# Performance work log

Measured on AMD Instinct MI355X. Metric: run time of the kernel, lower is better.

## Reference

```python
import jax, jax.numpy as jnp
import numpy as np

N = 100000      # nodes
E = 1600000     # edges (avg degree 16)
F_IN = 64       # num_features
HID = 16        # hidden channels (fixed in module)
OUT = 32        # num_classes
K = 2           # kernel_size (dim=1, degree=1 open B-spline -> 2 basis fns)


def setup_inputs() -> dict:
    key = jax.random.key(0)
    ks = jax.random.split(key, 8)
    return {
        "x": jax.random.normal(ks[0], (N, F_IN), jnp.float32),
        "edge_index": jax.random.randint(ks[1], (2, E), 0, N, dtype=jnp.int64),
        "dropout": 0,  # unused in eval mode (F.dropout training=False)
        "edge_attr": jnp.full((E, 1), 0.1, jnp.float32),  # nt([0.1]) broadcast per edge
        "W1": jax.random.normal(ks[2], (K, F_IN, HID), jnp.float32) / np.sqrt(K * F_IN).astype(np.float32),
        "root1": jax.random.normal(ks[3], (F_IN, HID), jnp.float32) / np.sqrt(F_IN).astype(np.float32),
        "bias1": jnp.zeros((HID,), jnp.float32),
        "W2": jax.random.normal(ks[4], (K, HID, OUT), jnp.float32) / np.sqrt(K * HID).astype(np.float32),
        "root2": jax.random.normal(ks[5], (HID, OUT), jnp.float32) / np.sqrt(HID).astype(np.float32),
        "bias2": jnp.zeros((OUT,), jnp.float32),
    }


def spline_conv(x, edge_index, edge_attr, W, root, bias):
    """SplineConv, dim=1, kernel_size=2, degree=1 open B-spline, aggr='mean'."""
    src, dst = edge_index[0], edge_index[1]
    n = x.shape[0]
    u = edge_attr[:, 0]                                  # [E] pseudo-coords in [0,1]
    # degree-1 open spline, kernel_size=2: frac = u*(ks-1) = u; kernels {0,1}
    basis = jnp.stack([1.0 - u, u], axis=1)              # [E, K]
    # transform at node level (cheaper than gathering raw features per edge)
    h = jnp.einsum('nf,kfo->nko', x, W)                  # [N, K, out]
    msg = jnp.einsum('ek,eko->eo', basis, h[src])        # [E, out]
    summed = jax.ops.segment_sum(msg, dst, num_segments=n)
    deg = jax.ops.segment_sum(jnp.ones_like(u), dst, num_segments=n)
    out = summed / jnp.maximum(deg, 1.0)[:, None]        # mean aggregation
    return out + x @ root + bias                          # root weight + bias


def reference(x, edge_index, dropout, edge_attr, W1, root1, bias1, W2, root2, bias2):
    # dropout is a no-op in eval mode
    h = jax.nn.elu(spline_conv(x, edge_index, edge_attr, W1, root1, bias1))
    h = spline_conv(h, edge_index, edge_attr, W2, root2, bias2)
    return jax.nn.log_softmax(h, axis=1)
```

## Files before the change

### kernel.cpp

```cpp
#include <hip/hip_runtime.h>
#include <math.h>

#define NN 100000
#define NE 1600000
#define F_IN 64
#define HID 16
#define OUTF 32
#define BKT_SHIFT 6
#define BKT_NODES 64
#define NBKT 1563
#define SRCM 0x1FFFF
#define CAP_REG 2048
#define CAP_LDS 1536
#define PBLK2 512
#define EPB2 (NE / PBLK2)
#define OVF_MAX 4096

__device__ __forceinline__ unsigned bf16r(float f) {
    unsigned u = __float_as_uint(f);
    return (u + 0x7FFFu + ((u >> 16) & 1u)) >> 16;
}
__device__ __forceinline__ float bfa(unsigned p) { return __uint_as_float(p << 16); }
__device__ __forceinline__ float bfd(unsigned p) { return __uint_as_float(p & 0xFFFF0000u); }
__device__ __forceinline__ float bfh(unsigned short v) { return __uint_as_float(((unsigned)v) << 16); }

__global__ __launch_bounds__(256) void zeroG_kernel(int* __restrict__ gcur,
                                                    int* __restrict__ novf) {
    int t = blockIdx.x * 256 + threadIdx.x;
    if (t < NBKT) gcur[t] = 0;
    if (t == NBKT) novf[0] = 0;
}

__global__ __launch_bounds__(1024) void partF_kernel(const int* __restrict__ ei,
                                                     const float* __restrict__ ea,
                                                     int* __restrict__ gcur,
                                                     int* __restrict__ novf,
                                                     int4* __restrict__ ovf,
                                                     int2* __restrict__ bkt) {
    __shared__ int hcnt[NBKT];
    __shared__ int hbase[NBKT];
    __shared__ int lbase[NBKT];
    __shared__ int s[1024];
    __shared__ int2 sbuf[EPB2];
    __shared__ unsigned short bid[EPB2];
    int t = threadIdx.x, blk = blockIdx.x;
    for (int i = t; i < NBKT; i += 1024) hcnt[i] = 0;
    __syncthreads();
    int beg = blk * EPB2, end = beg + EPB2;
    for (int e = beg + t; e < end; e += 1024)
        atomicAdd(&hcnt[ei[NE + e] >> BKT_SHIFT], 1);
    __syncthreads();
    int i0 = 2 * t, i1 = 2 * t + 1;
    int v0 = (i0 < NBKT) ? hcnt[i0] : 0;
    int v1 = (i1 < NBKT) ? hcnt[i1] : 0;
    s[t] = v0 + v1;
    __syncthreads();
    for (int off = 1; off < 1024; off <<= 1) {
        int xv = (t >= off) ? s[t - off] : 0;
        __syncthreads();
        s[t] += xv;
        __syncthreads();
    }
    int run = (t == 0) ? 0 : s[t - 1];
    if (i0 < NBKT) lbase[i0] = run;
    if (i1 < NBKT) lbase[i1] = run + v0;
    __syncthreads();
    for (int i = t; i < NBKT; i += 1024) {
        int c = hcnt[i];
        hbase[i] = c ? atomicAdd(&gcur[i], c) : 0;
        hcnt[i] = 0;
    }
    __syncthreads();
    for (int e = beg + t; e < end; e += 1024) {
        int src = ei[e];
        int dst = ei[NE + e];
        float u = ea[e];
        int b = dst >> BKT_SHIFT;
        int r = atomicAdd(&hcnt[b], 1);
        int lp = lbase[b] + r;
        sbuf[lp] = make_int2(src | ((dst & (BKT_NODES - 1)) << 17), __float_as_int(u));
        bid[lp] = (unsigned short)b;
    }
    __syncthreads();
    for (int i = t; i < EPB2; i += 1024) {
        int2 pk = sbuf[i];
        int b = bid[i];
        int p = hbase[b] + (i - lbase[b]);
        if (p < CAP_REG) {
            bkt[(size_t)b * CAP_REG + p] = pk;
        } else {
            int o = atomicAdd(novf, 1);
            if (o < OVF_MAX)
                ovf[o] = make_int4(b * BKT_NODES + (pk.x >> 17), pk.x & SRCM, pk.y, 0);
        }
    }
}

__global__ __launch_bounds__(256) void proj1_kernel(const float* __restrict__ x,
                                                    const float* __restrict__ W1,
                                                    const float* __restrict__ root1,
                                                    const float* __restrict__ bias1,
                                                    unsigned* __restrict__ ab1p,
                                                    float* __restrict__ r1) {
    __shared__ float w[2 * F_IN * HID];
    __shared__ float wr[F_IN * HID];
    __shared__ float bb[HID];
    for (int i = threadIdx.x; i < 2 * F_IN * HID; i += 256) w[i] = W1[i];
    for (int i = threadIdx.x; i < F_IN * HID; i += 256) wr[i] = root1[i];
    if (threadIdx.x < HID) bb[threadIdx.x] = bias1[threadIdx.x];
    __syncthreads();
    int n = blockIdx.x * 256 + threadIdx.x;
    if (n >= NN) return;
    float accA[HID], accB[HID], accR[HID];
#pragma unroll
    for (int o = 0; o < HID; ++o) { accA[o] = 0.f; accB[o] = 0.f; accR[o] = bb[o]; }
    const float* xr = x + (size_t)n * F_IN;
    for (int f = 0; f < F_IN; ++f) {
        float xv = xr[f];
        const float* w0 = &w[f * HID];
        const float* w1 = &w[F_IN * HID + f * HID];
        const float* w2 = &wr[f * HID];
#pragma unroll
        for (int o = 0; o < HID; ++o) {
            accA[o] = fmaf(xv, w0[o], accA[o]);
            accB[o] = fmaf(xv, w1[o], accB[o]);
            accR[o] = fmaf(xv, w2[o], accR[o]);
        }
    }
    unsigned* ar = ab1p + (size_t)n * HID;
    float* rr = r1 + (size_t)n * HID;
#pragma unroll
    for (int o = 0; o < HID; ++o) {
        ar[o] = bf16r(accA[o]) | (bf16r(accB[o] - accA[o]) << 16);
        rr[o] = accR[o];
    }
}

__global__ __launch_bounds__(512) void gather1_kernel(const int* __restrict__ gcur,
                                                      const int* __restrict__ novf,
                                                      const int4* __restrict__ ovf,
                                                      int2* __restrict__ bkt,
                                                      const unsigned* __restrict__ ab1p,
                                                      const float* __restrict__ r1,
                                                      unsigned short* __restrict__ h16,
                                                      float* __restrict__ dinv,
                                                      int* __restrict__ segg) {
    __shared__ int2 raw[CAP_LDS];
    __shared__ int2 sorted[CAP_LDS];
    __shared__ int cnt[BKT_NODES], cur[BKT_NODES], segb[BKT_NODES + 1];
    __shared__ float degsL[BKT_NODES];
    int t = threadIdx.x;
    int b = blockIdx.x;
    int tot = gcur[b];
    int beg = b * CAP_REG;
    if (t < BKT_NODES) { cnt[t] = 0; cur[t] = 0; degsL[t] = 0.f; }
    __syncthreads();
    int nodeBase = b * BKT_NODES;

    if (tot <= CAP_LDS) {
        for (int e = t; e < tot; e += 512) raw[e] = bkt[beg + e];
        __syncthreads();
        for (int e = t; e < tot; e += 512)
            atomicAdd(&cnt[((unsigned)raw[e].x) >> 17], 1);
        __syncthreads();
        if (t < BKT_NODES) {
            int v = cnt[t];
            int sc = v;
#pragma unroll
            for (int off = 1; off < 64; off <<= 1) {
                int o = __shfl_up(sc, off, 64);
                if (t >= off) sc += o;
            }
            segb[t] = sc - v;
            if (t == 63) segb[64] = sc;
        }
        __syncthreads();
        for (int e = t; e < tot; e += 512) {
            int2 pk = raw[e];
            int loc = ((unsigned)pk.x) >> 17;
            int pos = segb[loc] + atomicAdd(&cur[loc], 1);
            sorted[pos] = pk;
        }
        __syncthreads();
        for (int e = t; e < tot; e += 512) bkt[beg + e] = sorted[e];
        if (t <= BKT_NODES) segg[b * (BKT_NODES + 1) + t] = segb[t];
        int j = t & (HID - 1);
        int g = t >> 4;
        int s = segb[2 * g], mid = segb[2 * g + 1], e2 = segb[2 * g + 2];
        float a0 = 0.f, a1 = 0.f;
        int e = s;
        for (; e + 8 <= mid; e += 8) {
            float val[8];
#pragma unroll
            for (int k = 0; k < 8; ++k) {
                int2 pk = sorted[e + k];
                unsigned p = ab1p[(size_t)(pk.x & SRCM) * HID + j];
                val[k] = fmaf(__int_as_float(pk.y), bfd(p), bfa(p));
            }
#pragma unroll
            for (int k = 0; k < 8; ++k) a0 += val[k];
        }
        for (; e < mid; ++e) {
            int2 pk = sorted[e];
            unsigned p = ab1p[(size_t)(pk.x & SRCM) * HID + j];
            a0 += fmaf(__int_as_float(pk.y), bfd(p), bfa(p));
        }
        for (; e + 8 <= e2; e += 8) {
            float val[8];
#pragma unroll
            for (int k = 0; k < 8; ++k) {
                int2 pk = sorted[e + k];
                unsigned p = ab1p[(size_t)(pk.x & SRCM) * HID + j];
                val[k] = fmaf(__int_as_float(pk.y), bfd(p), bfa(p));
            }
#pragma unroll
            for (int k = 0; k < 8; ++k) a1 += val[k];
        }
        for (; e < e2; ++e) {
            int2 pk = sorted[e];
            unsigned p = ab1p[(size_t)(pk.x & SRCM) * HID + j];
            a1 += fmaf(__int_as_float(pk.y), bfd(p), bfa(p));
        }
        float d0 = 1.f / (float)max(mid - s, 1);
        float d1 = 1.f / (float)max(e2 - mid, 1);
        int n0 = nodeBase + 2 * g, n1 = n0 + 1;
        if (n0 < NN) {
            float v = a0 * d0 + r1[(size_t)n0 * HID + j];
            h16[(size_t)n0 * HID + j] = (unsigned short)bf16r(v > 0.f ? v : expm1f(v));
            if (j == 0) dinv[n0] = d0;
        }
        if (n1 < NN) {
            float v = a1 * d1 + r1[(size_t)n1 * HID + j];
            h16[(size_t)n1 * HID + j] = (unsigned short)bf16r(v > 0.f ? v : expm1f(v));
            if (j == 0) dinv[n1] = d1;
        }
    } else {
        float* accL = (float*)raw;
        int inreg = min(tot, CAP_REG);
        int end = beg + inreg;
        for (int i = t; i < BKT_NODES * HID; i += 512) accL[i] = 0.f;
        __syncthreads();
        int j = t & (HID - 1);
        int g = t >> 4;
        for (int e = beg + g; e < end; e += 32) {
            int2 pk = bkt[e];
            unsigned p = ab1p[(size_t)(pk.x & SRCM) * HID + j];
            atomicAdd(&accL[(((unsigned)pk.x) >> 17) * HID + j],
                      fmaf(__int_as_float(pk.y), bfd(p), bfa(p)));
            if (j == 0) atomicAdd(&degsL[((unsigned)pk.x) >> 17], 1.f);
        }
        int ovn = min(novf[0], OVF_MAX);
        for (int o = 0; o < ovn; ++o) {
            int4 ent = ovf[o];
            int loc = ent.x - nodeBase;
            if (loc >= 0 && loc < BKT_NODES && g == 0) {
                unsigned p = ab1p[(size_t)ent.y * HID + j];
                atomicAdd(&accL[loc * HID + j], fmaf(__int_as_float(ent.z), bfd(p), bfa(p)));
                if (j == 0) atomicAdd(&degsL[loc], 1.f);
            }
        }
        __syncthreads();
        if (t < BKT_NODES) degsL[t] = 1.f / fmaxf(degsL[t], 1.f);
        if (t == 0) segg[b * (BKT_NODES + 1)] = -1;
        __syncthreads();
#pragma unroll
        for (int it = 0; it < BKT_NODES * HID / 512; ++it) {
            int idx = it * 512 + t;
            int nl = idx >> 4, jj = idx & (HID - 1);
            int n = nodeBase + nl;
            if (n < NN) {
                float v = accL[idx] * degsL[nl] + r1[(size_t)n * HID + jj];
                h16[(size_t)n * HID + jj] = (unsigned short)bf16r(v > 0.f ? v : expm1f(v));
            }
        }
        if (t < BKT_NODES && nodeBase + t < NN) dinv[nodeBase + t] = degsL[t];
    }
}

__global__ __launch_bounds__(512) void gather2_kernel(const int* __restrict__ gcur,
                                                      const int* __restrict__ novf,
                                                      const int4* __restrict__ ovf,
                                                      const int2* __restrict__ bkt,
                                                      const unsigned short* __restrict__ h16,
                                                      const float* __restrict__ W2,
                                                      const float* __restrict__ root2,
                                                      const float* __restrict__ bias2,
                                                      const float* __restrict__ dinv,
                                                      const int* __restrict__ segg,
                                                      float* __restrict__ out) {
    __shared__ int2 sbufL[CAP_LDS];
    __shared__ int segb[BKT_NODES + 1];
    __shared__ float s0L[BKT_NODES * HID];
    __shared__ float s1L[BKT_NODES * HID];
    __shared__ float w20[HID * OUTF], w2d[HID * OUTF], wr[HID * OUTF];
    __shared__ float bb[OUTF];
    int t = threadIdx.x;
    for (int i = t; i < HID * OUTF; i += 512) {
        float a = W2[i];
        w20[i] = a;
        w2d[i] = W2[HID * OUTF + i] - a;
        wr[i] = root2[i];
    }
    if (t < OUTF) bb[t] = bias2[t];
    int b = blockIdx.x;
    int tot = gcur[b];
    int beg = b * CAP_REG;
    int nodeBase = b * BKT_NODES;
    if (t <= BKT_NODES) segb[t] = segg[b * (BKT_NODES + 1) + t];
    __syncthreads();

    if (tot <= CAP_LDS && segb[0] != -1) {
        for (int e = t; e < tot; e += 512) sbufL[e] = bkt[beg + e];
        __syncthreads();
        int j = t & (HID - 1);
        int g = t >> 4;
        int s = segb[2 * g], mid = segb[2 * g + 1], e2 = segb[2 * g + 2];
        float s00 = 0.f, s10 = 0.f, s01 = 0.f, s11 = 0.f;
        int e = s;
        for (; e + 8 <= mid; e += 8) {
            float hv[8], uv[8];
#pragma unroll
            for (int k = 0; k < 8; ++k) {
                int2 pk = sbufL[e + k];
                hv[k] = bfh(h16[(size_t)(pk.x & SRCM) * HID + j]);
                uv[k] = __int_as_float(pk.y);
            }
#pragma unroll
            for (int k = 0; k < 8; ++k) {
                s00 += hv[k];
                s10 = fmaf(uv[k], hv[k], s10);
            }
        }
        for (; e < mid; ++e) {
            int2 pk = sbufL[e];
            float hvv = bfh(h16[(size_t)(pk.x & SRCM) * HID + j]);
            s00 += hvv;
            s10 = fmaf(__int_as_float(pk.y), hvv, s10);
        }
        for (; e + 8 <= e2; e += 8) {
            float hv[8], uv[8];
#pragma unroll
            for (int k = 0; k < 8; ++k) {
                int2 pk = sbufL[e + k];
                hv[k] = bfh(h16[(size_t)(pk.x & SRCM) * HID + j]);
                uv[k] = __int_as_float(pk.y);
            }
#pragma unroll
            for (int k = 0; k < 8; ++k) {
                s01 += hv[k];
                s11 = fmaf(uv[k], hv[k], s11);
            }
        }
        for (; e < e2; ++e) {
            int2 pk = sbufL[e];
            float hvv = bfh(h16[(size_t)(pk.x & SRCM) * HID + j]);
            s01 += hvv;
            s11 = fmaf(__int_as_float(pk.y), hvv, s11);
        }
        s0L[(2 * g) * HID + j] = s00;
        s1L[(2 * g) * HID + j] = s10;
        s0L[(2 * g + 1) * HID + j] = s01;
        s1L[(2 * g + 1) * HID + j] = s11;
        __syncthreads();
    } else {
        int inreg = min(tot, CAP_REG);
        int end = beg + inreg;
        for (int i = t; i < BKT_NODES * HID; i += 512) { s0L[i] = 0.f; s1L[i] = 0.f; }
        __syncthreads();
        int j = t & (HID - 1);
        int g = t >> 4;
        for (int e = beg + g; e < end; e += 32) {
            int2 pk = bkt[e];
            float hvv = bfh(h16[(size_t)(pk.x & SRCM) * HID + j]);
            int l = ((unsigned)pk.x) >> 17;
            atomicAdd(&s0L[l * HID + j], hvv);
            atomicAdd(&s1L[l * HID + j], __int_as_float(pk.y) * hvv);
        }
        int ovn = min(novf[0], OVF_MAX);
        for (int o = 0; o < ovn; ++o) {
            int4 ent = ovf[o];
            int loc = ent.x - nodeBase;
            if (loc >= 0 && loc < BKT_NODES && g == 0) {
                float hvv = bfh(h16[(size_t)ent.y * HID + j]);
                atomicAdd(&s0L[loc * HID + j], hvv);
                atomicAdd(&s1L[loc * HID + j], __int_as_float(ent.z) * hvv);
            }
        }
        __syncthreads();
    }

#pragma unroll
    for (int it = 0; it < BKT_NODES * OUTF / 512; ++it) {
        int idx = it * 512 + t;
        int nl = idx >> 5, jj = idx & (OUTF - 1);
        int n = nodeBase + nl;
        float v = 0.f;
        if (n < NN) {
            float msum = 0.f;
            const float* S0 = &s0L[nl * HID];
            const float* S1 = &s1L[nl * HID];
#pragma unroll
            for (int f = 0; f < HID; ++f)
                msum += S0[f] * w20[f * OUTF + jj] + S1[f] * w2d[f * OUTF + jj];
            v = msum * dinv[n] + bb[jj];
            const unsigned short* hr = h16 + (size_t)n * HID;
#pragma unroll
            for (int f = 0; f < HID; ++f)
                v = fmaf(bfh(hr[f]), wr[f * OUTF + jj], v);
        }
        float m = v;
#pragma unroll
        for (int mask = 16; mask >= 1; mask >>= 1) m = fmaxf(m, __shfl_xor(m, mask));
        float ex = expf(v - m);
        float sm = ex;
#pragma unroll
        for (int mask = 16; mask >= 1; mask >>= 1) sm += __shfl_xor(sm, mask);
        if (n < NN) out[(size_t)n * OUTF + jj] = v - m - logf(sm);
    }
}

extern "C" void kernel_launch(void* const* d_in, const int* in_sizes, int n_in,
                              void* d_out, int out_size, void* d_ws, size_t ws_size,
                              hipStream_t stream) {
    const float* x     = (const float*)d_in[0];
    const int*   ei    = (const int*)d_in[1];
    const float* ea    = (const float*)d_in[3];
    const float* W1    = (const float*)d_in[4];
    const float* root1 = (const float*)d_in[5];
    const float* bias1 = (const float*)d_in[6];
    const float* W2    = (const float*)d_in[7];
    const float* root2 = (const float*)d_in[8];
    const float* bias2 = (const float*)d_in[9];
    float* out = (float*)d_out;
    float* ws  = (float*)d_ws;

    const size_t N = NN;
    int*            gcur = (int*)(ws);
    int*            novf = (int*)(ws + 2000);
    int4*           ovf  = (int4*)(ws + 2048);
    float*          dinv = ws + 20000;
    int*            segg = (int*)(ws + 120000);
    float*          r1   = ws + 222000;
    unsigned*       ab1p = (unsigned*)(ws + 222000 + 16 * N);
    unsigned short* h16  = (unsigned short*)(ws + 222000 + 32 * N);
    int2*           bkt  = (int2*)(ws + 222000 + 40 * N);

    int nbN = (NN + 255) / 256;
    zeroG_kernel<<<(NBKT + 256) / 256, 256, 0, stream>>>(gcur, novf);
    partF_kernel<<<PBLK2, 1024, 0, stream>>>(ei, ea, gcur, novf, ovf, bkt);
    proj1_kernel<<<nbN, 256, 0, stream>>>(x, W1, root1, bias1, ab1p, r1);
    gather1_kernel<<<NBKT, 512, 0, stream>>>(gcur, novf, ovf, bkt, ab1p, r1, h16, dinv, segg);
    gather2_kernel<<<NBKT, 512, 0, stream>>>(gcur, novf, ovf, bkt, h16, W2, root2, bias2, dinv, segg, out);
}
```

Before: 127.3 us.

## Vectorize edge loads and gathers, remap threads to per-node lanes

Partition blocks now use 500 blocks of 3200 edges so each thread loads four edges with int4/float4 vector reads. The projection kernel reads x rows as float4. Both gather kernels are remapped so that groups of 8 threads cover one node and each thread loads 4 or 8 packed bf16 features per edge as uint4, then combines partial sums with shuffles. Layer-2 self features are staged in LDS once per bucket. The aim is fewer, wider memory transactions on the irregular gathers, at the cost of shuffle reductions and possible lane imbalance on nodes with few edges.

```diff
diff --git a/kernel.cpp b/kernel.cpp
--- a/kernel.cpp
+++ b/kernel.cpp
@@ -12,8 +12,8 @@
 #define SRCM 0x1FFFF
 #define CAP_REG 2048
 #define CAP_LDS 1536
-#define PBLK2 512
-#define EPB2 (NE / PBLK2)
+#define PBLK2 500
+#define EPB2 3200
 #define OVF_MAX 4096
 
 __device__ __forceinline__ unsigned bf16r(float f) {
@@ -23,6 +23,23 @@
 __device__ __forceinline__ float bfa(unsigned p) { return __uint_as_float(p << 16); }
 __device__ __forceinline__ float bfd(unsigned p) { return __uint_as_float(p & 0xFFFF0000u); }
 __device__ __forceinline__ float bfh(unsigned short v) { return __uint_as_float(((unsigned)v) << 16); }
+
+__device__ __forceinline__ void acc8(uint4 hv, float u, float* s0, float* s1) {
+    unsigned w[4] = {hv.x, hv.y, hv.z, hv.w};
+#pragma unroll
+    for (int q = 0; q < 4; ++q) {
+        float lo = __uint_as_float(w[q] << 16);
+        float hi = __uint_as_float(w[q] & 0xFFFF0000u);
+        s0[2 * q]     += lo; s1[2 * q]     = fmaf(u, lo, s1[2 * q]);
+        s0[2 * q + 1] += hi; s1[2 * q + 1] = fmaf(u, hi, s1[2 * q + 1]);
+    }
+}
+__device__ __forceinline__ void acc4(uint4 ap, float u, float* a) {
+    unsigned w[4] = {ap.x, ap.y, ap.z, ap.w};
+#pragma unroll
+    for (int q = 0; q < 4; ++q)
+        a[q] += fmaf(u, bfd(w[q]), bfa(w[q]));
+}
 
 __global__ __launch_bounds__(256) void zeroG_kernel(int* __restrict__ gcur,
                                                     int* __restrict__ novf) {
@@ -46,9 +63,16 @@
     int t = threadIdx.x, blk = blockIdx.x;
     for (int i = t; i < NBKT; i += 1024) hcnt[i] = 0;
     __syncthreads();
-    int beg = blk * EPB2, end = beg + EPB2;
-    for (int e = beg + t; e < end; e += 1024)
-        atomicAdd(&hcnt[ei[NE + e] >> BKT_SHIFT], 1);
+    int beg = blk * EPB2;
+    int4 d4 = make_int4(0, 0, 0, 0);
+    bool act = (4 * t) < EPB2;
+    if (act) {
+        d4 = *(const int4*)(ei + NE + beg + 4 * t);
+        atomicAdd(&hcnt[d4.x >> BKT_SHIFT], 1);
+        atomicAdd(&hcnt[d4.y >> BKT_SHIFT], 1);
+        atomicAdd(&hcnt[d4.z >> BKT_SHIFT], 1);
+        atomicAdd(&hcnt[d4.w >> BKT_SHIFT], 1);
+    }
     __syncthreads();
     int i0 = 2 * t, i1 = 2 * t + 1;
     int v0 = (i0 < NBKT) ? hcnt[i0] : 0;
@@ -71,15 +95,21 @@
         hcnt[i] = 0;
     }
     __syncthreads();
-    for (int e = beg + t; e < end; e += 1024) {
-        int src = ei[e];
-        int dst = ei[NE + e];
-        float u = ea[e];
-        int b = dst >> BKT_SHIFT;
-        int r = atomicAdd(&hcnt[b], 1);
-        int lp = lbase[b] + r;
-        sbuf[lp] = make_int2(src | ((dst & (BKT_NODES - 1)) << 17), __float_as_int(u));
-        bid[lp] = (unsigned short)b;
+    if (act) {
+        int4 s4 = *(const int4*)(ei + beg + 4 * t);
+        float4 u4 = *(const float4*)(ea + beg + 4 * t);
+        int dst[4] = {d4.x, d4.y, d4.z, d4.w};
+        int src[4] = {s4.x, s4.y, s4.z, s4.w};
+        float uu[4] = {u4.x, u4.y, u4.z, u4.w};
+#pragma unroll
+        for (int k = 0; k < 4; ++k) {
+            int b = dst[k] >> BKT_SHIFT;
+            int r = atomicAdd(&hcnt[b], 1);
+            int lp = lbase[b] + r;
+            sbuf[lp] = make_int2(src[k] | ((dst[k] & (BKT_NODES - 1)) << 17),
+                                 __float_as_int(uu[k]));
+            bid[lp] = (unsigned short)b;
+        }
     }
     __syncthreads();
     for (int i = t; i < EPB2; i += 1024) {
@@ -91,7 +121,7 @@
         } else {
             int o = atomicAdd(novf, 1);
             if (o < OVF_MAX)
-                ovf[o] = make_int4(b * BKT_NODES + (pk.x >> 17), pk.x & SRCM, pk.y, 0);
+                ovf[o] = make_int4(b * BKT_NODES + (((unsigned)pk.x) >> 17), pk.x & SRCM, pk.y, 0);
         }
     }
 }
@@ -114,17 +144,23 @@
     float accA[HID], accB[HID], accR[HID];
 #pragma unroll
     for (int o = 0; o < HID; ++o) { accA[o] = 0.f; accB[o] = 0.f; accR[o] = bb[o]; }
-    const float* xr = x + (size_t)n * F_IN;
-    for (int f = 0; f < F_IN; ++f) {
-        float xv = xr[f];
-        const float* w0 = &w[f * HID];
-        const float* w1 = &w[F_IN * HID + f * HID];
-        const float* w2 = &wr[f * HID];
-#pragma unroll
-        for (int o = 0; o < HID; ++o) {
-            accA[o] = fmaf(xv, w0[o], accA[o]);
-            accB[o] = fmaf(xv, w1[o], accB[o]);
-            accR[o] = fmaf(xv, w2[o], accR[o]);
+    const float4* xr4 = (const float4*)(x + (size_t)n * F_IN);
+    for (int f4 = 0; f4 < F_IN / 4; ++f4) {
+        float4 xv4 = xr4[f4];
+        float xs[4] = {xv4.x, xv4.y, xv4.z, xv4.w};
+#pragma unroll
+        for (int q = 0; q < 4; ++q) {
+            int f = f4 * 4 + q;
+            float xv = xs[q];
+            const float* w0 = &w[f * HID];
+            const float* w1 = &w[F_IN * HID + f * HID];
+            const float* w2 = &wr[f * HID];
+#pragma unroll
+            for (int o = 0; o < HID; ++o) {
+                accA[o] = fmaf(xv, w0[o], accA[o]);
+                accB[o] = fmaf(xv, w1[o], accB[o]);
+                accR[o] = fmaf(xv, w2[o], accR[o]);
+            }
         }
     }
     unsigned* ar = ab1p + (size_t)n * HID;
@@ -184,55 +220,43 @@
         __syncthreads();
         for (int e = t; e < tot; e += 512) bkt[beg + e] = sorted[e];
         if (t <= BKT_NODES) segg[b * (BKT_NODES + 1) + t] = segb[t];
-        int j = t & (HID - 1);
-        int g = t >> 4;
-        int s = segb[2 * g], mid = segb[2 * g + 1], e2 = segb[2 * g + 2];
-        float a0 = 0.f, a1 = 0.f;
-        int e = s;
-        for (; e + 8 <= mid; e += 8) {
-            float val[8];
-#pragma unroll
-            for (int k = 0; k < 8; ++k) {
-                int2 pk = sorted[e + k];
-                unsigned p = ab1p[(size_t)(pk.x & SRCM) * HID + j];
-                val[k] = fmaf(__int_as_float(pk.y), bfd(p), bfa(p));
-            }
-#pragma unroll
-            for (int k = 0; k < 8; ++k) a0 += val[k];
-        }
-        for (; e < mid; ++e) {
+        int node = t >> 3;
+        int sub = (t >> 2) & 1;
+        int jq = t & 3;
+        int s0 = segb[node], e2 = segb[node + 1];
+        float acc[4] = {0.f, 0.f, 0.f, 0.f};
+        int e = s0 + sub;
+        for (; e + 2 < e2; e += 4) {
+            int2 pkA = sorted[e];
+            int2 pkB = sorted[e + 2];
+            uint4 apA = *(const uint4*)(ab1p + ((size_t)(pkA.x & SRCM) << 4) + (jq << 2));
+            uint4 apB = *(const uint4*)(ab1p + ((size_t)(pkB.x & SRCM) << 4) + (jq << 2));
+            acc4(apA, __int_as_float(pkA.y), acc);
+            acc4(apB, __int_as_float(pkB.y), acc);
+        }
+        if (e < e2) {
             int2 pk = sorted[e];
-            unsigned p = ab1p[(size_t)(pk.x & SRCM) * HID + j];
-            a0 += fmaf(__int_as_float(pk.y), bfd(p), bfa(p));
-        }
-        for (; e + 8 <= e2; e += 8) {
-            float val[8];
-#pragma unroll
-            for (int k = 0; k < 8; ++k) {
-                int2 pk = sorted[e + k];
-                unsigned p = ab1p[(size_t)(pk.x & SRCM) * HID + j];
-                val[k] = fmaf(__int_as_float(pk.y), bfd(p), bfa(p));
-            }
-#pragma unroll
-            for (int k = 0; k < 8; ++k) a1 += val[k];
-        }
-        for (; e < e2; ++e) {
-            int2 pk = sorted[e];
-            unsigned p = ab1p[(size_t)(pk.x & SRCM) * HID + j];
-            a1 += fmaf(__int_as_float(pk.y), bfd(p), bfa(p));
-        }
-        float d0 = 1.f / (float)max(mid - s, 1);
-        float d1 = 1.f / (float)max(e2 - mid, 1);
-        int n0 = nodeBase + 2 * g, n1 = n0 + 1;
-        if (n0 < NN) {
-            float v = a0 * d0 + r1[(size_t)n0 * HID + j];
-            h16[(size_t)n0 * HID + j] = (unsigned short)bf16r(v > 0.f ? v : expm1f(v));
-            if (j == 0) dinv[n0] = d0;
-        }
-        if (n1 < NN) {
-            float v = a1 * d1 + r1[(size_t)n1 * HID + j];
-            h16[(size_t)n1 * HID + j] = (unsigned short)bf16r(v > 0.f ? v : expm1f(v));
-            if (j == 0) dinv[n1] = d1;
+            uint4 ap = *(const uint4*)(ab1p + ((size_t)(pk.x & SRCM) << 4) + (jq << 2));
+            acc4(ap, __int_as_float(pk.y), acc);
+        }
+#pragma unroll
+        for (int k = 0; k < 4; ++k) acc[k] += __shfl_xor(acc[k], 4);
+        if (sub == 0) {
+            int n = nodeBase + node;
+            if (n < NN) {
+                float d0 = 1.f / (float)max(e2 - s0, 1);
+                float4 rv = *(const float4*)(r1 + ((size_t)n << 4) + (jq << 2));
+                float rr[4] = {rv.x, rv.y, rv.z, rv.w};
+                unsigned hw[4];
+#pragma unroll
+                for (int k = 0; k < 4; ++k) {
+                    float v = acc[k] * d0 + rr[k];
+                    hw[k] = bf16r(v > 0.f ? v : expm1f(v));
+                }
+                *(uint2*)(h16 + ((size_t)n << 4) + (jq << 2)) =
+                    make_uint2(hw[0] | (hw[1] << 16), hw[2] | (hw[3] << 16));
+                if (jq == 0) dinv[n] = d0;
+            }
         }
     } else {
         float* accL = (float*)raw;
@@ -292,6 +316,7 @@
     __shared__ int segb[BKT_NODES + 1];
     __shared__ float s0L[BKT_NODES * HID];
     __shared__ float s1L[BKT_NODES * HID];
+    __shared__ float hloc[BKT_NODES * HID];
     __shared__ float w20[HID * OUTF], w2d[HID * OUTF], wr[HID * OUTF];
     __shared__ float bb[OUTF];
     int t = threadIdx.x;
@@ -307,60 +332,45 @@
     int beg = b * CAP_REG;
     int nodeBase = b * BKT_NODES;
     if (t <= BKT_NODES) segb[t] = segg[b * (BKT_NODES + 1) + t];
+    for (int i = t; i < BKT_NODES * HID; i += 512) {
+        int n = nodeBase + (i >> 4);
+        hloc[i] = (n < NN) ? bfh(h16[((size_t)nodeBase << 4) + i]) : 0.f;
+    }
     __syncthreads();
 
     if (tot <= CAP_LDS && segb[0] != -1) {
         for (int e = t; e < tot; e += 512) sbufL[e] = bkt[beg + e];
         __syncthreads();
-        int j = t & (HID - 1);
-        int g = t >> 4;
-        int s = segb[2 * g], mid = segb[2 * g + 1], e2 = segb[2 * g + 2];
-        float s00 = 0.f, s10 = 0.f, s01 = 0.f, s11 = 0.f;
-        int e = s;
-        for (; e + 8 <= mid; e += 8) {
-            float hv[8], uv[8];
-#pragma unroll
-            for (int k = 0; k < 8; ++k) {
-                int2 pk = sbufL[e + k];
-                hv[k] = bfh(h16[(size_t)(pk.x & SRCM) * HID + j]);
-                uv[k] = __int_as_float(pk.y);
-            }
-#pragma unroll
-            for (int k = 0; k < 8; ++k) {
-                s00 += hv[k];
-                s10 = fmaf(uv[k], hv[k], s10);
-            }
-        }
-        for (; e < mid; ++e) {
+        int node = t >> 3;
+        int sub = (t >> 1) & 3;
+        int jh = t & 1;
+        int s = segb[node], e2 = segb[node + 1];
+        float s0[8] = {0.f, 0.f, 0.f, 0.f, 0.f, 0.f, 0.f, 0.f};
+        float s1[8] = {0.f, 0.f, 0.f, 0.f, 0.f, 0.f, 0.f, 0.f};
+        int e = s + sub;
+        for (; e + 4 < e2; e += 8) {
+            int2 pkA = sbufL[e];
+            int2 pkB = sbufL[e + 4];
+            uint4 hvA = *(const uint4*)(h16 + ((size_t)(pkA.x & SRCM) << 4) + (jh << 3));
+            uint4 hvB = *(const uint4*)(h16 + ((size_t)(pkB.x & SRCM) << 4) + (jh << 3));
+            acc8(hvA, __int_as_float(pkA.y), s0, s1);
+            acc8(hvB, __int_as_float(pkB.y), s0, s1);
+        }
+        if (e < e2) {
             int2 pk = sbufL[e];
-            float hvv = bfh(h16[(size_t)(pk.x & SRCM) * HID + j]);
-            s00 += hvv;
-            s10 = fmaf(__int_as_float(pk.y), hvv, s10);
-        }
-        for (; e + 8 <= e2; e += 8) {
-            float hv[8], uv[8];
-#pragma unroll
-            for (int k = 0; k < 8; ++k) {
-                int2 pk = sbufL[e + k];
-                hv[k] = bfh(h16[(size_t)(pk.x & SRCM) * HID + j]);
-                uv[k] = __int_as_float(pk.y);
-            }
-#pragma unroll
-            for (int k = 0; k < 8; ++k) {
-                s01 += hv[k];
-                s11 = fmaf(uv[k], hv[k], s11);
-            }
-        }
-        for (; e < e2; ++e) {
-            int2 pk = sbufL[e];
-            float hvv = bfh(h16[(size_t)(pk.x & SRCM) * HID + j]);
-            s01 += hvv;
-            s11 = fmaf(__int_as_float(pk.y), hvv, s11);
-        }
-        s0L[(2 * g) * HID + j] = s00;
-        s1L[(2 * g) * HID + j] = s10;
-        s0L[(2 * g + 1) * HID + j] = s01;
-        s1L[(2 * g + 1) * HID + j] = s11;
+            uint4 hv = *(const uint4*)(h16 + ((size_t)(pk.x & SRCM) << 4) + (jh << 3));
+            acc8(hv, __int_as_float(pk.y), s0, s1);
+        }
+#pragma unroll
+        for (int k = 0; k < 8; ++k) {
+            s0[k] += __shfl_xor(s0[k], 2); s0[k] += __shfl_xor(s0[k], 4);
+            s1[k] += __shfl_xor(s1[k], 2); s1[k] += __shfl_xor(s1[k], 4);
+        }
+        if (sub == 0) {
+            int base = node * HID + jh * 8;
+#pragma unroll
+            for (int k = 0; k < 8; ++k) { s0L[base + k] = s0[k]; s1L[base + k] = s1[k]; }
+        }
         __syncthreads();
     } else {
         int inreg = min(tot, CAP_REG);
@@ -403,10 +413,10 @@
             for (int f = 0; f < HID; ++f)
                 msum += S0[f] * w20[f * OUTF + jj] + S1[f] * w2d[f * OUTF + jj];
             v = msum * dinv[n] + bb[jj];
-            const unsigned short* hr = h16 + (size_t)n * HID;
+            const float* hr = &hloc[nl * HID];
 #pragma unroll
             for (int f = 0; f < HID; ++f)
-                v = fmaf(bfh(hr[f]), wr[f * OUTF + jj], v);
+                v = fmaf(hr[f], wr[f * OUTF + jj], v);
         }
         float m = v;
 #pragma unroll
```

Result: faster. 119.8 us (-5.9%).
